# Kernel optimization log

Hardware: AMD Instinct MI355X
Metric: run time of the kernel (lower is better)

The kernel has to match this reference:

```python
import jax, jax.numpy as jnp
import numpy as np

D = 1024
HEADS = 16
LN_EPS = 1e-5   # torch LayerNorm default
SHEP_EPS = 1e-4 # eps in shepards_MHA
SHEP_P = 2


def setup_inputs() -> dict:
    key = jax.random.key(0)
    k1, k2, k3 = jax.random.split(key, 3)
    b, t, d = 2, 2048, D
    X = jax.random.normal(k1, (b, t, d), dtype=jnp.float32)
    # Linear weights, scaled like torch default init (~U(-1/sqrt(fan_in), ...)) magnitude
    W_in = jax.random.normal(k2, (4 * d, d), dtype=jnp.float32) * (1.0 / np.sqrt(d))
    b_in = jnp.zeros((4 * d,), dtype=jnp.float32)
    W_out = jax.random.normal(k3, (d, d), dtype=jnp.float32) * (1.0 / np.sqrt(d))
    b_out = jnp.zeros((d,), dtype=jnp.float32)
    return {"X": X, "W_in": W_in, "b_in": b_in, "W_out": W_out, "b_out": b_out}


def _shepards_mha(Q, K, V):
    # Q,K,V: [b,h,t,dh]. Euclidean cdist via ||q||^2 + ||k||^2 - 2 q.k
    q2 = jnp.sum(Q * Q, axis=-1, keepdims=True)          # [b,h,t,1]
    k2 = jnp.sum(K * K, axis=-1, keepdims=True)          # [b,h,t,1]
    sq = q2 + jnp.swapaxes(k2, -1, -2) - 2.0 * jnp.einsum('bhqd,bhkd->bhqk', Q, K)
    dist = jnp.sqrt(jnp.maximum(sq, 0.0))                # [b,h,t,t]
    W = (SHEP_EPS + dist) ** (-SHEP_P)
    W = W / (SHEP_EPS + jnp.sum(W, axis=-1, keepdims=True))
    return jnp.einsum('bhqk,bhkd->bhqd', W, V)


def reference(X, W_in, b_in, W_out, b_out):
    b, t, d = X.shape
    h = HEADS
    dh = d // h
    # LayerNorm (no affine)
    mu = jnp.mean(X, axis=-1, keepdims=True)
    var = jnp.mean((X - mu) ** 2, axis=-1, keepdims=True)
    Xn = (X - mu) / jnp.sqrt(var + LN_EPS)
    # project_in: [b,t,4d]
    P = jnp.einsum('btd,ed->bte', Xn, W_in) + b_in
    # [b,t,h,4*dh] -> [b,h,t,4*dh]
    P = P.reshape(b, t, h, 4 * dh).transpose(0, 2, 1, 3)
    Q, K, V, G = jnp.split(P, 4, axis=-1)                # each [b,h,t,dh]
    A = _shepards_mha(Q, K, V)
    O = (G * A).transpose(0, 2, 1, 3).reshape(b, t, d)
    return X + jnp.einsum('btd,ed->bte', O, W_out) + b_out
```

## Files before the change

### kernel.cpp

```cpp
#include <hip/hip_runtime.h>

#define SEQ 2048
#define D_MODEL 1024
#define NTOK 4096
#define PROW 4096
#define DH 64
#define LN_EPS 1e-5f
#define SHEP_EPS 1e-4f

typedef __attribute__((ext_vector_type(8))) short bf16x8;
typedef __attribute__((ext_vector_type(4))) short s16x4;
typedef __attribute__((ext_vector_type(4))) float f32x4;

__device__ __forceinline__ unsigned short f2bf(float f) {
  union { float f; unsigned u; } v; v.f = f;
  unsigned r = v.u + 0x7fffu + ((v.u >> 16) & 1u);
  return (unsigned short)(r >> 16);
}
__device__ __forceinline__ float bf2f(unsigned short s) {
  union { unsigned u; float f; } v; v.u = ((unsigned)s) << 16;
  return v.f;
}
__device__ __forceinline__ void gload16(const void* g, void* l) {
  __builtin_amdgcn_global_load_lds(
      (const __attribute__((address_space(1))) unsigned int*)g,
      (__attribute__((address_space(3))) unsigned int*)l, 16, 0, 0);
}
__device__ __forceinline__ void gload4(const void* g, void* l) {
  __builtin_amdgcn_global_load_lds(
      (const __attribute__((address_space(1))) unsigned int*)g,
      (__attribute__((address_space(3))) unsigned int*)l, 4, 0, 0);
}
__device__ __forceinline__ unsigned cvt_pk_bf16(float lo, float hi) {
  unsigned r;
  asm("v_cvt_pk_bf16_f32 %0, %1, %2" : "=v"(r) : "v"(lo), "v"(hi));
  return r;
}
#define MFMA16(a, b, c) __builtin_amdgcn_mfma_f32_16x16x32_bf16(a, b, c, 0, 0, 0)

__global__ __launch_bounds__(256) void ln_kernel(const float* __restrict__ X,
                                                 unsigned short* __restrict__ Xn) {
  int row = blockIdx.x, tid = threadIdx.x;
  const float4* xr = (const float4*)(X + (size_t)row * D_MODEL);
  float4 v = xr[tid];
  float s = v.x + v.y + v.z + v.w;
  float s2 = v.x * v.x + v.y * v.y + v.z * v.z + v.w * v.w;
#pragma unroll
  for (int off = 32; off > 0; off >>= 1) {
    s += __shfl_down(s, off);
    s2 += __shfl_down(s2, off);
  }
  __shared__ float red[8];
  __shared__ float mb[2];
  int wv = tid >> 6;
  if ((tid & 63) == 0) { red[wv] = s; red[4 + wv] = s2; }
  __syncthreads();
  if (tid == 0) {
    float ts = red[0] + red[1] + red[2] + red[3];
    float t2 = red[4] + red[5] + red[6] + red[7];
    float mu = ts * (1.f / D_MODEL);
    float var = t2 * (1.f / D_MODEL) - mu * mu;
    mb[0] = mu;
    mb[1] = rsqrtf(var + LN_EPS);
  }
  __syncthreads();
  float mu = mb[0], rs = mb[1];
  s16x4 o;
  o[0] = (short)f2bf((v.x - mu) * rs);
  o[1] = (short)f2bf((v.y - mu) * rs);
  o[2] = (short)f2bf((v.z - mu) * rs);
  o[3] = (short)f2bf((v.w - mu) * rs);
  ((s16x4*)(Xn + (size_t)row * D_MODEL))[tid] = o;
}

__global__ __launch_bounds__(256) void cvt_bf16_kernel(const float* __restrict__ in,
                                                       unsigned short* __restrict__ out,
                                                       int n4) {
  int i = blockIdx.x * 256 + threadIdx.x;
  if (i >= n4) return;
  float4 v = ((const float4*)in)[i];
  s16x4 o;
  o[0] = (short)f2bf(v.x);
  o[1] = (short)f2bf(v.y);
  o[2] = (short)f2bf(v.z);
  o[3] = (short)f2bf(v.w);
  ((s16x4*)out)[i] = o;
}

__global__ __launch_bounds__(256) void gemm_p_kernel(
    const unsigned short* __restrict__ A, const unsigned short* __restrict__ B,
    const float* __restrict__ bias, unsigned short* __restrict__ C,
    int M, int N, int K) {
  __shared__ __align__(16) unsigned short sA[128 * 32];
  __shared__ __align__(16) unsigned short sB[128 * 32];
  int tid = threadIdx.x;
  int m0 = blockIdx.y * 128, n0 = blockIdx.x * 128;
  int wv = tid >> 6, lane = tid & 63;
  int wr = wv >> 1, wc = wv & 1;
  int lr = lane & 15, lq = lane >> 4;
  f32x4 acc[4][4] = {};
  int srow = tid >> 2, scol = (tid & 3) * 8;
  const unsigned short* gA = A + (size_t)(m0 + srow) * K + scol;
  const unsigned short* gB = B + (size_t)(n0 + srow) * K + scol;
  unsigned short* lA = sA + tid * 8;
  unsigned short* lB = sB + tid * 8;
  for (int k0 = 0; k0 < K; k0 += 32) {
    gload16(gA + k0, lA);
    gload16(gA + k0 + (size_t)64 * K, lA + 64 * 32);
    gload16(gB + k0, lB);
    gload16(gB + k0 + (size_t)64 * K, lB + 64 * 32);
    __syncthreads();
    bf16x8 af[4], bfr[4];
#pragma unroll
    for (int m = 0; m < 4; m++)
      af[m] = *(const bf16x8*)&sA[(wr * 64 + m * 16 + lr) * 32 + lq * 8];
#pragma unroll
    for (int n = 0; n < 4; n++)
      bfr[n] = *(const bf16x8*)&sB[(wc * 64 + n * 16 + lr) * 32 + lq * 8];
#pragma unroll
    for (int m = 0; m < 4; m++)
#pragma unroll
      for (int n = 0; n < 4; n++)
        acc[m][n] = MFMA16(af[m], bfr[n], acc[m][n]);
    __syncthreads();
  }
#pragma unroll
  for (int m = 0; m < 4; m++) {
    int row = m0 + wr * 64 + m * 16 + lq * 4;
#pragma unroll
    for (int n = 0; n < 4; n++) {
      int col = n0 + wc * 64 + n * 16 + lr;
      float bv = bias[col];
#pragma unroll
      for (int r = 0; r < 4; r++)
        C[(size_t)(row + r) * N + col] = f2bf(acc[m][n][r] + bv);
    }
  }
}

__global__ __launch_bounds__(256) void gemm_out_kernel(
    const unsigned short* __restrict__ A, const unsigned short* __restrict__ B,
    const float* __restrict__ bias, const float* __restrict__ Xres,
    float* __restrict__ Out, int M, int N, int K) {
  __shared__ __align__(16) unsigned short sA[128 * 32];
  __shared__ __align__(16) unsigned short sB[128 * 32];
  int tid = threadIdx.x;
  int m0 = blockIdx.y * 128, n0 = blockIdx.x * 128;
  int wv = tid >> 6, lane = tid & 63;
  int wr = wv >> 1, wc = wv & 1;
  int lr = lane & 15, lq = lane >> 4;
  f32x4 acc[4][4] = {};
  int srow = tid >> 2, scol = (tid & 3) * 8;
  const unsigned short* gA = A + (size_t)(m0 + srow) * K + scol;
  const unsigned short* gB = B + (size_t)(n0 + srow) * K + scol;
  unsigned short* lA = sA + tid * 8;
  unsigned short* lB = sB + tid * 8;
  for (int k0 = 0; k0 < K; k0 += 32) {
    gload16(gA + k0, lA);
    gload16(gA + k0 + (size_t)64 * K, lA + 64 * 32);
    gload16(gB + k0, lB);
    gload16(gB + k0 + (size_t)64 * K, lB + 64 * 32);
    __syncthreads();
    bf16x8 af[4], bfr[4];
#pragma unroll
    for (int m = 0; m < 4; m++)
      af[m] = *(const bf16x8*)&sA[(wr * 64 + m * 16 + lr) * 32 + lq * 8];
#pragma unroll
    for (int n = 0; n < 4; n++)
      bfr[n] = *(const bf16x8*)&sB[(wc * 64 + n * 16 + lr) * 32 + lq * 8];
#pragma unroll
    for (int m = 0; m < 4; m++)
#pragma unroll
      for (int n = 0; n < 4; n++)
        acc[m][n] = MFMA16(af[m], bfr[n], acc[m][n]);
    __syncthreads();
  }
#pragma unroll
  for (int m = 0; m < 4; m++) {
    int row = m0 + wr * 64 + m * 16 + lq * 4;
#pragma unroll
    for (int n = 0; n < 4; n++) {
      int col = n0 + wc * 64 + n * 16 + lr;
      float bv = bias[col];
#pragma unroll
      for (int r = 0; r < 4; r++) {
        size_t idx = (size_t)(row + r) * N + col;
        Out[idx] = Xres[idx] + acc[m][n][r] + bv;
      }
    }
  }
}

__global__ __launch_bounds__(256) void transv_kernel(const unsigned short* __restrict__ P,
                                                     unsigned short* __restrict__ Vt) {
  int kt = blockIdx.x;
  int bh = blockIdx.y;
  int b = bh >> 4, h = bh & 15;
  __shared__ unsigned short sT[64][72];
  int tid = threadIdx.x;
  const unsigned short* vbase = P + ((size_t)(b * SEQ + kt * 64)) * PROW + h * 256 + 128;
#pragma unroll
  for (int it = 0; it < 2; it++) {
    int c = tid + it * 256;
    int k = c >> 3, c0 = (c & 7) * 8;
    uint4 u = *(const uint4*)(vbase + (size_t)k * PROW + c0);
    unsigned e[4] = {u.x, u.y, u.z, u.w};
#pragma unroll
    for (int j = 0; j < 4; j++) {
      sT[c0 + 2 * j][k] = (unsigned short)(e[j] & 0xffffu);
      sT[c0 + 2 * j + 1][k] = (unsigned short)(e[j] >> 16);
    }
  }
  __syncthreads();
  unsigned short* obase = Vt + (size_t)bh * 64 * SEQ + kt * 64;
#pragma unroll
  for (int it = 0; it < 2; it++) {
    int cc = tid + it * 256;
    int crow = cc >> 3, k0 = (cc & 7) * 8;
    uint4 o;
    unsigned short e[8];
#pragma unroll
    for (int j = 0; j < 8; j++) e[j] = sT[crow][k0 + j];
    o.x = (unsigned)e[0] | ((unsigned)e[1] << 16);
    o.y = (unsigned)e[2] | ((unsigned)e[3] << 16);
    o.z = (unsigned)e[4] | ((unsigned)e[5] << 16);
    o.w = (unsigned)e[6] | ((unsigned)e[7] << 16);
    *(uint4*)(obase + (size_t)crow * SEQ + k0) = o;
  }
}

__global__ __launch_bounds__(256) void norms_kernel(const unsigned short* __restrict__ P,
                                                    float* __restrict__ nrm) {
  int id = blockIdx.x * 256 + threadIdx.x;
  int bh = id >> 12;
  int which = (id >> 11) & 1;
  int t = id & 2047;
  int b = bh >> 4, h = bh & 15;
  const unsigned short* p = P + ((size_t)(b * SEQ + t)) * PROW + h * 256 + which * 64;
  const uint4* pv = (const uint4*)p;
  float acc = 0.f;
#pragma unroll
  for (int i = 0; i < 8; i++) {
    uint4 u = pv[i];
    unsigned arr[4] = {u.x, u.y, u.z, u.w};
#pragma unroll
    for (int j = 0; j < 4; j++) {
      float lo = __uint_as_float(arr[j] << 16);
      float hi = __uint_as_float(arr[j] & 0xffff0000u);
      acc += lo * lo + hi * hi;
    }
  }
  nrm[(size_t)(bh * 2 + which) * SEQ + t] = acc;
}

__global__ __launch_bounds__(512) void attn_kernel(
    const unsigned short* __restrict__ P, const unsigned short* __restrict__ Vt,
    const float* __restrict__ nrm, unsigned short* __restrict__ O) {
  int qt = blockIdx.x, bh = blockIdx.y;
  int b = bh >> 4, h = bh & 15;
  int tid = threadIdx.x;
  int w = tid >> 6, lane = tid & 63;
  int lr = lane & 15, lq = lane >> 4;

  __shared__ __align__(16) unsigned short sQ[128 * 64];
  __shared__ __align__(16) unsigned short sK[2][64 * 64];
  __shared__ __align__(16) unsigned short sV[2][64 * 64];
  __shared__ __align__(16) unsigned short sW[128 * 64];
  __shared__ __align__(16) float sK2[2][64];
  __shared__ __align__(16) float sDen[8][16];

  const unsigned short* qbase = P + ((size_t)(b * SEQ + qt * 128)) * PROW + h * 256;
  const unsigned short* kbase = P + ((size_t)(b * SEQ)) * PROW + h * 256 + 64;
  const unsigned short* vtb = Vt + (size_t)bh * 64 * SEQ;
  const float* k2base = nrm + (size_t)(bh * 2 + 1) * SEQ;

  int srow = tid >> 3;
  int scol = ((tid & 7) ^ (srow & 7)) * 8;
  const unsigned short* kSrc = kbase + (size_t)srow * PROW + scol;
  const unsigned short* vSrc = vtb + (size_t)srow * SEQ + scol;

#pragma unroll
  for (int it = 0; it < 2; it++) {
    int c = tid + it * 512;
    int row = c >> 3;
    int col = ((c & 7) ^ (row & 7)) * 8;
    gload16(qbase + (size_t)row * PROW + col, (char*)sQ + c * 16);
  }
  gload16(kSrc, (char*)&sK[0][0] + tid * 16);
  gload16(vSrc, (char*)&sV[0][0] + tid * 16);
  if (w == 0) gload4(k2base + lane, (char*)&sK2[0][0] + lane * 4);
  float q2 = nrm[(size_t)(bh * 2) * SEQ + qt * 128 + 16 * w + lr];
  __syncthreads();

  int qrow = 16 * w + lr;
  bf16x8 qf[2];
#pragma unroll
  for (int ks = 0; ks < 2; ks++)
    qf[ks] = *(const bf16x8*)((const char*)sQ + qrow * 128 +
                              ((ks * 64 + lq * 16) ^ ((lr & 7) << 4)));

  f32x4 num[4] = {};
  float den = 0.f;
  char* wrow = (char*)sW + qrow * 128;

  for (int kt = 0; kt < SEQ / 64; kt++) {
    int cur = kt & 1, nxt = cur ^ 1;
    if (kt < SEQ / 64 - 1) {
      gload16(kSrc + (size_t)(kt + 1) * 64 * PROW, (char*)&sK[nxt][0] + tid * 16);
      gload16(vSrc + (size_t)(kt + 1) * 64, (char*)&sV[nxt][0] + tid * 16);
      if (w == 0) gload4(k2base + (kt + 1) * 64 + lane, (char*)&sK2[nxt][0] + lane * 4);
    }

    f32x4 st[4] = {};
#pragma unroll
    for (int fk = 0; fk < 4; fk++) {
      int row = 16 * fk + lr;
      const char* krow = (const char*)&sK[cur][0] + row * 128;
      bf16x8 kf0 = *(const bf16x8*)(krow + ((lq * 16) ^ ((row & 7) << 4)));
      bf16x8 kf1 = *(const bf16x8*)(krow + ((64 + lq * 16) ^ ((row & 7) << 4)));
      st[fk] = MFMA16(kf0, qf[0], st[fk]);
      st[fk] = MFMA16(kf1, qf[1], st[fk]);
    }

#pragma unroll
    for (int fk = 0; fk < 4; fk++) {
      f32x4 k2v = *(const f32x4*)&sK2[cur][16 * fk + 4 * lq];
      float w0 = __builtin_amdgcn_rcpf(fmaxf(fmaf(-2.f, st[fk][0], q2 + k2v[0]), 1e-8f));
      float w1 = __builtin_amdgcn_rcpf(fmaxf(fmaf(-2.f, st[fk][1], q2 + k2v[1]), 1e-8f));
      float w2 = __builtin_amdgcn_rcpf(fmaxf(fmaf(-2.f, st[fk][2], q2 + k2v[2]), 1e-8f));
      float w3 = __builtin_amdgcn_rcpf(fmaxf(fmaf(-2.f, st[fk][3], q2 + k2v[3]), 1e-8f));
      den += (w0 + w1) + (w2 + w3);
      uint2 pp;
      pp.x = cvt_pk_bf16(w0, w1);
      pp.y = cvt_pk_bf16(w2, w3);
      *(uint2*)(wrow + ((32 * fk + 8 * lq) ^ ((lr & 7) << 4))) = pp;
    }

#pragma unroll
    for (int ks = 0; ks < 2; ks++) {
      bf16x8 aw = *(const bf16x8*)(wrow + ((64 * ks + 16 * lq) ^ ((lr & 7) << 4)));
#pragma unroll
      for (int fn = 0; fn < 4; fn++) {
        int row = 16 * fn + lr;
        bf16x8 bv = *(const bf16x8*)((const char*)&sV[cur][0] + row * 128 +
                                     ((64 * ks + 16 * lq) ^ ((row & 7) << 4)));
        num[fn] = MFMA16(aw, bv, num[fn]);
      }
    }
    __syncthreads();
  }

  den += __shfl_xor(den, 16);
  den += __shfl_xor(den, 32);
  if (lq == 0) sDen[w][lr] = den;
  __syncthreads();
  f32x4 dv = *(const f32x4*)&sDen[w][4 * lq];
  f32x4 rdv;
#pragma unroll
  for (int r = 0; r < 4; r++) rdv[r] = __builtin_amdgcn_rcpf(dv[r] + SHEP_EPS);

  const unsigned short* gbase = qbase + 192;
#pragma unroll
  for (int fn = 0; fn < 4; fn++) {
    int c = 16 * fn + lr;
#pragma unroll
    for (int r = 0; r < 4; r++) {
      int ql = 16 * w + 4 * lq + r;
      float g = bf2f(gbase[(size_t)ql * PROW + c]);
      float a = num[fn][r] * rdv[r];
      O[((size_t)(b * SEQ + qt * 128 + ql)) * D_MODEL + h * DH + c] = f2bf(g * a);
    }
  }
}

extern "C" void kernel_launch(void* const* d_in, const int* in_sizes, int n_in,
                              void* d_out, int out_size, void* d_ws, size_t ws_size,
                              hipStream_t stream) {
  const float* X = (const float*)d_in[0];
  const float* W_in = (const float*)d_in[1];
  const float* b_in = (const float*)d_in[2];
  const float* W_out = (const float*)d_in[3];
  const float* b_out = (const float*)d_in[4];
  float* out = (float*)d_out;

  char* ws = (char*)d_ws;
  unsigned short* Xn = (unsigned short*)(ws);
  unsigned short* O = (unsigned short*)(ws);
  unsigned short* Wi = (unsigned short*)(ws + ((size_t)8 << 20));
  unsigned short* Vt = (unsigned short*)(ws + ((size_t)8 << 20));
  unsigned short* Wo = (unsigned short*)(ws + ((size_t)16 << 20));
  unsigned short* P = (unsigned short*)(ws + ((size_t)18 << 20));
  float* nrm = (float*)(ws + ((size_t)50 << 20));

  ln_kernel<<<NTOK, 256, 0, stream>>>(X, Xn);
  cvt_bf16_kernel<<<4096, 256, 0, stream>>>(W_in, Wi, (4096 * 1024) / 4);
  cvt_bf16_kernel<<<1024, 256, 0, stream>>>(W_out, Wo, (1024 * 1024) / 4);
  gemm_p_kernel<<<dim3(32, 32), 256, 0, stream>>>(Xn, Wi, b_in, P, 4096, 4096, 1024);
  transv_kernel<<<dim3(32, 32), 256, 0, stream>>>(P, Vt);
  norms_kernel<<<512, 256, 0, stream>>>(P, nrm);
  attn_kernel<<<dim3(16, 32), 512, 0, stream>>>(P, Vt, nrm, O);
  gemm_out_kernel<<<dim3(8, 32), 256, 0, stream>>>(O, Wo, b_out, X, out, 4096, 1024, 1024);
}
```

Before: 170.8 us.

## Split attention key range across two wave groups in 1024-thread blocks

```diff
diff --git a/kernel.cpp b/kernel.cpp
--- a/kernel.cpp
+++ b/kernel.cpp
@@ -253,7 +253,7 @@
   nrm[(size_t)(bh * 2 + which) * SEQ + t] = acc;
 }
 
-__global__ __launch_bounds__(512) void attn_kernel(
+__global__ __launch_bounds__(1024, 8) void attn_kernel(
     const unsigned short* __restrict__ P, const unsigned short* __restrict__ Vt,
     const float* __restrict__ nrm, unsigned short* __restrict__ O) {
   int qt = blockIdx.x, bh = blockIdx.y;
@@ -261,70 +261,73 @@
   int tid = threadIdx.x;
   int w = tid >> 6, lane = tid & 63;
   int lr = lane & 15, lq = lane >> 4;
-
-  __shared__ __align__(16) unsigned short sQ[128 * 64];
-  __shared__ __align__(16) unsigned short sK[2][64 * 64];
-  __shared__ __align__(16) unsigned short sV[2][64 * 64];
-  __shared__ __align__(16) unsigned short sW[128 * 64];
+  int wg = w >> 3;
+  int wq = w & 7;
+
+  __shared__ __align__(16) unsigned short sQW[256 * 64];
+  __shared__ __align__(16) unsigned short sKV[2][2][64 * 64];
   __shared__ __align__(16) float sK2[2][64];
-  __shared__ __align__(16) float sDen[8][16];
+  __shared__ __align__(16) float sDen[16][16];
 
   const unsigned short* qbase = P + ((size_t)(b * SEQ + qt * 128)) * PROW + h * 256;
   const unsigned short* kbase = P + ((size_t)(b * SEQ)) * PROW + h * 256 + 64;
   const unsigned short* vtb = Vt + (size_t)bh * 64 * SEQ;
   const float* k2base = nrm + (size_t)(bh * 2 + 1) * SEQ;
 
-  int srow = tid >> 3;
-  int scol = ((tid & 7) ^ (srow & 7)) * 8;
+  int sg = wg;
+  int idx = tid & 511;
+  int srow = idx >> 3;
+  int scol = ((idx & 7) ^ (srow & 7)) * 8;
+  char* kdst = (char*)&sKV[0][sg][0] + idx * 16;
+  char* vdst = (char*)&sKV[1][sg][0] + idx * 16;
   const unsigned short* kSrc = kbase + (size_t)srow * PROW + scol;
   const unsigned short* vSrc = vtb + (size_t)srow * SEQ + scol;
 
-#pragma unroll
-  for (int it = 0; it < 2; it++) {
-    int c = tid + it * 512;
-    int row = c >> 3;
-    int col = ((c & 7) ^ (row & 7)) * 8;
-    gload16(qbase + (size_t)row * PROW + col, (char*)sQ + c * 16);
-  }
-  gload16(kSrc, (char*)&sK[0][0] + tid * 16);
-  gload16(vSrc, (char*)&sV[0][0] + tid * 16);
-  if (w == 0) gload4(k2base + lane, (char*)&sK2[0][0] + lane * 4);
-  float q2 = nrm[(size_t)(bh * 2) * SEQ + qt * 128 + 16 * w + lr];
+  {
+    int qrow_s = tid >> 3;
+    int qcol_s = ((tid & 7) ^ (qrow_s & 7)) * 8;
+    gload16(qbase + (size_t)qrow_s * PROW + qcol_s, (char*)sQW + tid * 16);
+  }
+  float q2 = nrm[(size_t)(bh * 2) * SEQ + qt * 128 + 16 * wq + lr];
   __syncthreads();
 
-  int qrow = 16 * w + lr;
+  int qrow = 16 * wq + lr;
   bf16x8 qf[2];
 #pragma unroll
   for (int ks = 0; ks < 2; ks++)
-    qf[ks] = *(const bf16x8*)((const char*)sQ + qrow * 128 +
+    qf[ks] = *(const bf16x8*)((const char*)sQW + qrow * 128 +
                               ((ks * 64 + lq * 16) ^ ((lr & 7) << 4)));
 
   f32x4 num[4] = {};
   float den = 0.f;
-  char* wrow = (char*)sW + qrow * 128;
-
-  for (int kt = 0; kt < SEQ / 64; kt++) {
-    int cur = kt & 1, nxt = cur ^ 1;
-    if (kt < SEQ / 64 - 1) {
-      gload16(kSrc + (size_t)(kt + 1) * 64 * PROW, (char*)&sK[nxt][0] + tid * 16);
-      gload16(vSrc + (size_t)(kt + 1) * 64, (char*)&sV[nxt][0] + tid * 16);
-      if (w == 0) gload4(k2base + (kt + 1) * 64 + lane, (char*)&sK2[nxt][0] + lane * 4);
-    }
+  char* wrow = (char*)sQW + (16 * w + lr) * 128;
+
+  for (int t = 0; t < SEQ / 128; t++) {
+    int kt = 2 * t + wg;
+    gload16(kSrc + (size_t)(2 * t + sg) * 64 * PROW, kdst);
+    gload16(vSrc + (size_t)(2 * t + sg) * 64, vdst);
+    if (tid < 128) {
+      int g2 = tid >> 6;
+      gload4(k2base + (2 * t + g2) * 64 + lane, (char*)&sK2[g2][0] + lane * 4);
+    }
+    __syncthreads();
 
     f32x4 st[4] = {};
+    __builtin_amdgcn_s_setprio(1);
 #pragma unroll
     for (int fk = 0; fk < 4; fk++) {
       int row = 16 * fk + lr;
-      const char* krow = (const char*)&sK[cur][0] + row * 128;
+      const char* krow = (const char*)&sKV[0][wg][0] + row * 128;
       bf16x8 kf0 = *(const bf16x8*)(krow + ((lq * 16) ^ ((row & 7) << 4)));
       bf16x8 kf1 = *(const bf16x8*)(krow + ((64 + lq * 16) ^ ((row & 7) << 4)));
       st[fk] = MFMA16(kf0, qf[0], st[fk]);
       st[fk] = MFMA16(kf1, qf[1], st[fk]);
     }
+    __builtin_amdgcn_s_setprio(0);
 
 #pragma unroll
     for (int fk = 0; fk < 4; fk++) {
-      f32x4 k2v = *(const f32x4*)&sK2[cur][16 * fk + 4 * lq];
+      f32x4 k2v = *(const f32x4*)&sK2[wg][16 * fk + 4 * lq];
       float w0 = __builtin_amdgcn_rcpf(fmaxf(fmaf(-2.f, st[fk][0], q2 + k2v[0]), 1e-8f));
       float w1 = __builtin_amdgcn_rcpf(fmaxf(fmaf(-2.f, st[fk][1], q2 + k2v[1]), 1e-8f));
       float w2 = __builtin_amdgcn_rcpf(fmaxf(fmaf(-2.f, st[fk][2], q2 + k2v[2]), 1e-8f));
@@ -336,39 +339,56 @@
       *(uint2*)(wrow + ((32 * fk + 8 * lq) ^ ((lr & 7) << 4))) = pp;
     }
 
+    __builtin_amdgcn_s_setprio(1);
 #pragma unroll
     for (int ks = 0; ks < 2; ks++) {
       bf16x8 aw = *(const bf16x8*)(wrow + ((64 * ks + 16 * lq) ^ ((lr & 7) << 4)));
 #pragma unroll
       for (int fn = 0; fn < 4; fn++) {
         int row = 16 * fn + lr;
-        bf16x8 bv = *(const bf16x8*)((const char*)&sV[cur][0] + row * 128 +
+        bf16x8 bv = *(const bf16x8*)((const char*)&sKV[1][wg][0] + row * 128 +
                                      ((64 * ks + 16 * lq) ^ ((row & 7) << 4)));
         num[fn] = MFMA16(aw, bv, num[fn]);
       }
     }
+    __builtin_amdgcn_s_setprio(0);
     __syncthreads();
   }
 
   den += __shfl_xor(den, 16);
   den += __shfl_xor(den, 32);
   if (lq == 0) sDen[w][lr] = den;
+  float* xch = (float*)&sKV[0][0][0];
+  if (wg == 1) {
+#pragma unroll
+    for (int fn = 0; fn < 4; fn++)
+      *(f32x4*)&xch[((size_t)(wq * 64 + lane)) * 16 + fn * 4] = num[fn];
+  }
   __syncthreads();
-  f32x4 dv = *(const f32x4*)&sDen[w][4 * lq];
-  f32x4 rdv;
-#pragma unroll
-  for (int r = 0; r < 4; r++) rdv[r] = __builtin_amdgcn_rcpf(dv[r] + SHEP_EPS);
-
-  const unsigned short* gbase = qbase + 192;
-#pragma unroll
-  for (int fn = 0; fn < 4; fn++) {
-    int c = 16 * fn + lr;
-#pragma unroll
-    for (int r = 0; r < 4; r++) {
-      int ql = 16 * w + 4 * lq + r;
-      float g = bf2f(gbase[(size_t)ql * PROW + c]);
-      float a = num[fn][r] * rdv[r];
-      O[((size_t)(b * SEQ + qt * 128 + ql)) * D_MODEL + h * DH + c] = f2bf(g * a);
+
+  if (wg == 0) {
+#pragma unroll
+    for (int fn = 0; fn < 4; fn++)
+      num[fn] += *(const f32x4*)&xch[((size_t)(wq * 64 + lane)) * 16 + fn * 4];
+
+    f32x4 dv = *(const f32x4*)&sDen[wq][4 * lq];
+    f32x4 dv2 = *(const f32x4*)&sDen[wq + 8][4 * lq];
+    f32x4 rdv;
+#pragma unroll
+    for (int r = 0; r < 4; r++)
+      rdv[r] = __builtin_amdgcn_rcpf(dv[r] + dv2[r] + SHEP_EPS);
+
+    const unsigned short* gbase = qbase + 192;
+#pragma unroll
+    for (int fn = 0; fn < 4; fn++) {
+      int c = 16 * fn + lr;
+#pragma unroll
+      for (int r = 0; r < 4; r++) {
+        int ql = 16 * wq + 4 * lq + r;
+        float g = bf2f(gbase[(size_t)ql * PROW + c]);
+        float a = num[fn][r] * rdv[r];
+        O[((size_t)(b * SEQ + qt * 128 + ql)) * D_MODEL + h * DH + c] = f2bf(g * a);
+      }
     }
   }
 }
@@ -398,6 +418,6 @@
   gemm_p_kernel<<<dim3(32, 32), 256, 0, stream>>>(Xn, Wi, b_in, P, 4096, 4096, 1024);
   transv_kernel<<<dim3(32, 32), 256, 0, stream>>>(P, Vt);
   norms_kernel<<<512, 256, 0, stream>>>(P, nrm);
-  attn_kernel<<<dim3(16, 32), 512, 0, stream>>>(P, Vt, nrm, O);
+  attn_kernel<<<dim3(16, 32), 1024, 0, stream>>>(P, Vt, nrm, O);
   gemm_out_kernel<<<dim3(8, 32), 256, 0, stream>>>(O, Wo, b_out, X, out, 4096, 1024, 1024);
 }
```

Result: slower. 178.5 us (+4.5%).

## Halve attention block to 4 warps, each handling two 16-row query fragments

Applied to the files above, without the earlier changes.

```diff
diff --git a/kernel.cpp b/kernel.cpp
--- a/kernel.cpp
+++ b/kernel.cpp
@@ -253,9 +253,10 @@
   nrm[(size_t)(bh * 2 + which) * SEQ + t] = acc;
 }
 
-__global__ __launch_bounds__(512) void attn_kernel(
+__global__ __launch_bounds__(256) void attn_kernel(
     const unsigned short* __restrict__ P, const unsigned short* __restrict__ Vt,
     const float* __restrict__ nrm, unsigned short* __restrict__ O) {
+  const int NT = SEQ / 64;
   int qt = blockIdx.x, bh = blockIdx.y;
   int b = bh >> 4, h = bh & 15;
   int tid = threadIdx.x;
@@ -267,108 +268,138 @@
   __shared__ __align__(16) unsigned short sV[2][64 * 64];
   __shared__ __align__(16) unsigned short sW[128 * 64];
   __shared__ __align__(16) float sK2[2][64];
-  __shared__ __align__(16) float sDen[8][16];
+  __shared__ __align__(16) float sDen[4][2][16];
 
   const unsigned short* qbase = P + ((size_t)(b * SEQ + qt * 128)) * PROW + h * 256;
   const unsigned short* kbase = P + ((size_t)(b * SEQ)) * PROW + h * 256 + 64;
   const unsigned short* vtb = Vt + (size_t)bh * 64 * SEQ;
   const float* k2base = nrm + (size_t)(bh * 2 + 1) * SEQ;
 
-  int srow = tid >> 3;
-  int scol = ((tid & 7) ^ (srow & 7)) * 8;
-  const unsigned short* kSrc = kbase + (size_t)srow * PROW + scol;
-  const unsigned short* vSrc = vtb + (size_t)srow * SEQ + scol;
-
-#pragma unroll
-  for (int it = 0; it < 2; it++) {
-    int c = tid + it * 512;
+  auto stage_kv = [&](int t, int buf) {
+#pragma unroll
+    for (int it = 0; it < 2; it++) {
+      int c = tid + it * 256;
+      int row = c >> 3;
+      int col = ((c & 7) ^ (row & 7)) * 8;
+      gload16(kbase + (size_t)(t * 64 + row) * PROW + col, (char*)&sK[buf][0] + c * 16);
+      gload16(vtb + (size_t)row * SEQ + t * 64 + col, (char*)&sV[buf][0] + c * 16);
+    }
+    if (tid < 64) gload4(k2base + t * 64 + tid, (char*)&sK2[buf][0] + tid * 4);
+  };
+
+#pragma unroll
+  for (int it = 0; it < 4; it++) {
+    int c = tid + it * 256;
     int row = c >> 3;
     int col = ((c & 7) ^ (row & 7)) * 8;
     gload16(qbase + (size_t)row * PROW + col, (char*)sQ + c * 16);
   }
-  gload16(kSrc, (char*)&sK[0][0] + tid * 16);
-  gload16(vSrc, (char*)&sV[0][0] + tid * 16);
-  if (w == 0) gload4(k2base + lane, (char*)&sK2[0][0] + lane * 4);
-  float q2 = nrm[(size_t)(bh * 2) * SEQ + qt * 128 + 16 * w + lr];
+  stage_kv(0, 0);
+  float q2f0 = nrm[(size_t)(bh * 2) * SEQ + qt * 128 + 32 * w + lr];
+  float q2f1 = nrm[(size_t)(bh * 2) * SEQ + qt * 128 + 32 * w + 16 + lr];
   __syncthreads();
 
-  int qrow = 16 * w + lr;
-  bf16x8 qf[2];
-#pragma unroll
-  for (int ks = 0; ks < 2; ks++)
-    qf[ks] = *(const bf16x8*)((const char*)sQ + qrow * 128 +
-                              ((ks * 64 + lq * 16) ^ ((lr & 7) << 4)));
-
-  f32x4 num[4] = {};
-  float den = 0.f;
-  char* wrow = (char*)sW + qrow * 128;
-
-  for (int kt = 0; kt < SEQ / 64; kt++) {
-    int cur = kt & 1, nxt = cur ^ 1;
-    if (kt < SEQ / 64 - 1) {
-      gload16(kSrc + (size_t)(kt + 1) * 64 * PROW, (char*)&sK[nxt][0] + tid * 16);
-      gload16(vSrc + (size_t)(kt + 1) * 64, (char*)&sV[nxt][0] + tid * 16);
-      if (w == 0) gload4(k2base + (kt + 1) * 64 + lane, (char*)&sK2[nxt][0] + lane * 4);
-    }
-
-    f32x4 st[4] = {};
+  bf16x8 qf[2][2];
+#pragma unroll
+  for (int fq = 0; fq < 2; fq++) {
+    int row = 32 * w + 16 * fq + lr;
+#pragma unroll
+    for (int ks = 0; ks < 2; ks++)
+      qf[fq][ks] = *(const bf16x8*)((const char*)sQ + row * 128 +
+                                    ((ks * 64 + lq * 16) ^ ((row & 7) << 4)));
+  }
+
+  f32x4 num[2][4] = {};
+  float den[2] = {0.f, 0.f};
+  char* wrow0 = (char*)sW + (32 * w + lr) * 128;
+  char* wrow1 = (char*)sW + (32 * w + 16 + lr) * 128;
+
+  for (int t = 0; t < NT; t++) {
+    int cur = t & 1;
+    if (t + 1 < NT) stage_kv(t + 1, cur ^ 1);
+
+    f32x4 st[2][4] = {};
+    __builtin_amdgcn_s_setprio(1);
 #pragma unroll
     for (int fk = 0; fk < 4; fk++) {
       int row = 16 * fk + lr;
       const char* krow = (const char*)&sK[cur][0] + row * 128;
       bf16x8 kf0 = *(const bf16x8*)(krow + ((lq * 16) ^ ((row & 7) << 4)));
       bf16x8 kf1 = *(const bf16x8*)(krow + ((64 + lq * 16) ^ ((row & 7) << 4)));
-      st[fk] = MFMA16(kf0, qf[0], st[fk]);
-      st[fk] = MFMA16(kf1, qf[1], st[fk]);
-    }
+      st[0][fk] = MFMA16(kf0, qf[0][0], st[0][fk]);
+      st[0][fk] = MFMA16(kf1, qf[0][1], st[0][fk]);
+      st[1][fk] = MFMA16(kf0, qf[1][0], st[1][fk]);
+      st[1][fk] = MFMA16(kf1, qf[1][1], st[1][fk]);
+    }
+    __builtin_amdgcn_s_setprio(0);
 
 #pragma unroll
     for (int fk = 0; fk < 4; fk++) {
       f32x4 k2v = *(const f32x4*)&sK2[cur][16 * fk + 4 * lq];
-      float w0 = __builtin_amdgcn_rcpf(fmaxf(fmaf(-2.f, st[fk][0], q2 + k2v[0]), 1e-8f));
-      float w1 = __builtin_amdgcn_rcpf(fmaxf(fmaf(-2.f, st[fk][1], q2 + k2v[1]), 1e-8f));
-      float w2 = __builtin_amdgcn_rcpf(fmaxf(fmaf(-2.f, st[fk][2], q2 + k2v[2]), 1e-8f));
-      float w3 = __builtin_amdgcn_rcpf(fmaxf(fmaf(-2.f, st[fk][3], q2 + k2v[3]), 1e-8f));
-      den += (w0 + w1) + (w2 + w3);
-      uint2 pp;
-      pp.x = cvt_pk_bf16(w0, w1);
-      pp.y = cvt_pk_bf16(w2, w3);
-      *(uint2*)(wrow + ((32 * fk + 8 * lq) ^ ((lr & 7) << 4))) = pp;
-    }
-
+#pragma unroll
+      for (int fq = 0; fq < 2; fq++) {
+        float q2 = fq ? q2f1 : q2f0;
+        float w0 = __builtin_amdgcn_rcpf(fmaxf(fmaf(-2.f, st[fq][fk][0], q2 + k2v[0]), 1e-8f));
+        float w1 = __builtin_amdgcn_rcpf(fmaxf(fmaf(-2.f, st[fq][fk][1], q2 + k2v[1]), 1e-8f));
+        float w2 = __builtin_amdgcn_rcpf(fmaxf(fmaf(-2.f, st[fq][fk][2], q2 + k2v[2]), 1e-8f));
+        float w3 = __builtin_amdgcn_rcpf(fmaxf(fmaf(-2.f, st[fq][fk][3], q2 + k2v[3]), 1e-8f));
+        den[fq] += (w0 + w1) + (w2 + w3);
+        uint2 pp;
+        pp.x = cvt_pk_bf16(w0, w1);
+        pp.y = cvt_pk_bf16(w2, w3);
+        char* wr = fq ? wrow1 : wrow0;
+        *(uint2*)(wr + ((32 * fk + 8 * lq) ^ ((lr & 7) << 4))) = pp;
+      }
+    }
+
+    __builtin_amdgcn_s_setprio(1);
 #pragma unroll
     for (int ks = 0; ks < 2; ks++) {
-      bf16x8 aw = *(const bf16x8*)(wrow + ((64 * ks + 16 * lq) ^ ((lr & 7) << 4)));
+      bf16x8 aw0 = *(const bf16x8*)(wrow0 + ((64 * ks + 16 * lq) ^ ((lr & 7) << 4)));
+      bf16x8 aw1 = *(const bf16x8*)(wrow1 + ((64 * ks + 16 * lq) ^ ((lr & 7) << 4)));
 #pragma unroll
       for (int fn = 0; fn < 4; fn++) {
         int row = 16 * fn + lr;
         bf16x8 bv = *(const bf16x8*)((const char*)&sV[cur][0] + row * 128 +
                                      ((64 * ks + 16 * lq) ^ ((row & 7) << 4)));
-        num[fn] = MFMA16(aw, bv, num[fn]);
+        num[0][fn] = MFMA16(aw0, bv, num[0][fn]);
+        num[1][fn] = MFMA16(aw1, bv, num[1][fn]);
       }
     }
+    __builtin_amdgcn_s_setprio(0);
+
     __syncthreads();
   }
 
-  den += __shfl_xor(den, 16);
-  den += __shfl_xor(den, 32);
-  if (lq == 0) sDen[w][lr] = den;
+#pragma unroll
+  for (int fq = 0; fq < 2; fq++) {
+    den[fq] += __shfl_xor(den[fq], 16);
+    den[fq] += __shfl_xor(den[fq], 32);
+  }
+  if (lq == 0) {
+    sDen[w][0][lr] = den[0];
+    sDen[w][1][lr] = den[1];
+  }
   __syncthreads();
-  f32x4 dv = *(const f32x4*)&sDen[w][4 * lq];
-  f32x4 rdv;
-#pragma unroll
-  for (int r = 0; r < 4; r++) rdv[r] = __builtin_amdgcn_rcpf(dv[r] + SHEP_EPS);
 
   const unsigned short* gbase = qbase + 192;
 #pragma unroll
-  for (int fn = 0; fn < 4; fn++) {
-    int c = 16 * fn + lr;
-#pragma unroll
-    for (int r = 0; r < 4; r++) {
-      int ql = 16 * w + 4 * lq + r;
-      float g = bf2f(gbase[(size_t)ql * PROW + c]);
-      float a = num[fn][r] * rdv[r];
-      O[((size_t)(b * SEQ + qt * 128 + ql)) * D_MODEL + h * DH + c] = f2bf(g * a);
+  for (int fq = 0; fq < 2; fq++) {
+    f32x4 dv = *(const f32x4*)&sDen[w][fq][4 * lq];
+    f32x4 rdv;
+#pragma unroll
+    for (int r = 0; r < 4; r++)
+      rdv[r] = __builtin_amdgcn_rcpf(dv[r] + SHEP_EPS);
+#pragma unroll
+    for (int fn = 0; fn < 4; fn++) {
+      int c = 16 * fn + lr;
+#pragma unroll
+      for (int r = 0; r < 4; r++) {
+        int ql = 32 * w + 16 * fq + 4 * lq + r;
+        float g = bf2f(gbase[(size_t)ql * PROW + c]);
+        O[((size_t)(b * SEQ + qt * 128 + ql)) * D_MODEL + h * DH + c] =
+            f2bf(g * num[fq][fn][r] * rdv[r]);
+      }
     }
   }
 }
@@ -398,6 +429,6 @@
   gemm_p_kernel<<<dim3(32, 32), 256, 0, stream>>>(Xn, Wi, b_in, P, 4096, 4096, 1024);
   transv_kernel<<<dim3(32, 32), 256, 0, stream>>>(P, Vt);
   norms_kernel<<<512, 256, 0, stream>>>(P, nrm);
-  attn_kernel<<<dim3(16, 32), 512, 0, stream>>>(P, Vt, nrm, O);
+  attn_kernel<<<dim3(16, 32), 256, 0, stream>>>(P, Vt, nrm, O);
   gemm_out_kernel<<<dim3(8, 32), 256, 0, stream>>>(O, Wo, b_out, X, out, 4096, 1024, 1024);
 }
```

New measurement: 173.9 us. Within noise of the previous version (+1.8%).
